# Performance work log

Hardware: AMD Instinct MI355X
Metric: run time of the kernel (lower is better)

## Reference

```python
import jax, jax.numpy as jnp
import numpy as np

G = 8            # grid_size
G2 = G * G       # total_grid_size = 64
NS = 2.0         # neighborhood_size
H = 64           # h_dim
A = 1024         # bottleneck_dim == attention_dim
S = 32           # number of sequences
N = 64           # pedestrians per sequence
P = 4096         # scene boundary points per sequence (down_samples)
B = S * N        # total batch = 2048


def setup_inputs() -> dict:
    key = jax.random.key(0)
    ks = jax.random.split(key, 16)
    starts = jnp.arange(S, dtype=jnp.int32) * N
    seq_start_end = jnp.stack([starts, starts + N], axis=1)  # (S, 2) uniform groups
    return {
        "h_states": jax.random.normal(ks[0], (1, B, H), jnp.float32),
        "end_pos": jax.random.normal(ks[1], (B, 2), jnp.float32),
        "rel_pos": jax.random.normal(ks[2], (B, 2), jnp.float32) * 0.1,
        "scene_info": jax.random.normal(ks[3], (S, P, 2), jnp.float32),
        # Attention_Decoder params (soft attention over G2 grid cells, encoder_dim=1)
        "W_enc": jax.random.normal(ks[4], (1, A), jnp.float32) * 0.05,
        "b_enc": jnp.zeros((A,), jnp.float32),
        "W_dec": jax.random.normal(ks[5], (H, A), jnp.float32) * 0.05,
        "b_dec": jnp.zeros((A,), jnp.float32),
        "w_full": jax.random.normal(ks[6], (A, 1), jnp.float32) * 0.05,
        "b_full": jnp.zeros((1,), jnp.float32),
        "W_out": jax.random.normal(ks[7], (1 + H + 4, A), jnp.float32) * 0.05,  # [ctx, h, embed_info]
        "b_out": jnp.zeros((A,), jnp.float32),
        # mlp_pool: Linear(A, A) + BatchNorm1d + ReLU
        "W_mlp": jax.random.normal(ks[8], (A, A), jnp.float32) * 0.05,
        "b_mlp": jnp.zeros((A,), jnp.float32),
        "gamma": jnp.ones((A,), jnp.float32),
        "beta": jnp.zeros((A,), jnp.float32),
        "seq_start_end": seq_start_end,
    }


def _occupancy(end_pos, scene_info, num_seqs, peds, grid_size, ns):
    """Vectorized per-pedestrian grid-cell binning + scatter-add occupancy.
    end_pos: (num_seqs*peds, 2), scene_info: (num_seqs, P, 2) -> (B, G2)."""
    g2 = grid_size * grid_size
    b = num_seqs * peds
    ep = end_pos.reshape(num_seqs, peds, 1, 2)
    sx = scene_info[:, None, :, 0]  # (S, 1, P)
    sy = scene_info[:, None, :, 1]
    tl_x = ep[..., 0] - ns / 2
    tl_y = ep[..., 1] + ns / 2
    br_x = ep[..., 0] + ns / 2
    br_y = ep[..., 1] - ns / 2
    cell_x = jnp.floor((sx - tl_x) / ns * grid_size)   # (S, N, P)
    cell_y = jnp.floor((tl_y - sy) / ns * grid_size)
    cell = (cell_x + cell_y * grid_size).astype(jnp.int32)
    # point is out-of-bound if outside the ped's neighborhood box (matches torch mask)
    oob = (sx >= br_x) | (sx <= tl_x) | (sy >= tl_y) | (sy <= br_y)
    ped = jnp.arange(b, dtype=jnp.int32).reshape(num_seqs, peds, 1)
    # torch scatters masked points into slot 0 then drops it; we use one dump slot at the end
    idx = jnp.where(oob, b * g2, ped * g2 + cell)      # (S, N, P)
    counts = jax.ops.segment_sum(
        jnp.ones(idx.size, jnp.float32), idx.reshape(-1), num_segments=b * g2 + 1)
    return counts[:-1].reshape(b, g2)


def reference(h_states, end_pos, rel_pos, scene_info,
              W_enc, b_enc, W_dec, b_dec, w_full, b_full,
              W_out, b_out, W_mlp, b_mlp, gamma, beta, seq_start_end):
    num_seqs = seq_start_end.shape[0]
    b = end_pos.shape[0]
    peds = b // num_seqs
    occ = _occupancy(end_pos, scene_info, num_seqs, peds, G, NS)   # (B, G2)
    enc = occ[..., None]                                           # (B, G2, 1)
    h = h_states.reshape(b, -1)                                    # (B, H)
    embed_info = jnp.concatenate([end_pos, rel_pos], axis=1)       # (B, 4)
    # soft attention over the G2 grid cells conditioned on the decoder hidden state
    att = jax.nn.relu(enc @ W_enc + b_enc + (h @ W_dec + b_dec)[:, None, :])  # (B, G2, A)
    e = (att @ w_full)[..., 0] + b_full                            # (B, G2)
    alpha = jax.nn.softmax(e, axis=1)
    ctx = jnp.sum(alpha[..., None] * enc, axis=1)                  # (B, 1)
    pool = jnp.concatenate([ctx, h, embed_info], axis=1) @ W_out + b_out  # (B, A)
    # mlp_pool: Linear -> BatchNorm1d (training stats, biased var) -> ReLU
    y = pool @ W_mlp + b_mlp
    mu = jnp.mean(y, axis=0)
    var = jnp.mean((y - mu) ** 2, axis=0)
    y = gamma * (y - mu) * jax.lax.rsqrt(var + 1e-5) + beta
    return jax.nn.relu(y)
```

## Files before the change

kernel.cpp:

```cpp
#include <hip/hip_runtime.h>
#include <hip/hip_bf16.h>


#define NPED 2048
#define NA   1024
#define NH   64
#define NG2  64
#define NPTS 4096

typedef unsigned short ushort_t;
typedef __attribute__((ext_vector_type(8))) short bf16x8;
typedef __attribute__((ext_vector_type(4))) float f32x4;

struct PrepPtrs { const void* p[15]; };

__device__ __forceinline__ float bf2f(ushort_t u) {
  return __uint_as_float(((unsigned int)u) << 16);
}
__device__ __forceinline__ ushort_t f2bf(float f) {
  __hip_bfloat16 b = __float2bfloat16(f);
  return *reinterpret_cast<ushort_t*>(&b);
}

__global__ void k_detect(const unsigned short* __restrict__ h, int* __restrict__ flag) {
  __shared__ int bad_sh;
  if (threadIdx.x == 0) bad_sh = 0;
  __syncthreads();
  int bad = 0;
  for (int i = threadIdx.x; i < 4096; i += 256) {
    float v = __uint_as_float(((unsigned int)h[i]) << 16);
    if (!(fabsf(v) <= 1e4f)) bad = 1;
  }
  if (bad) atomicOr(&bad_sh, 1);
  __syncthreads();
  if (threadIdx.x == 0) flag[0] = (bad_sh == 0) ? 1 : 0;
}

__device__ __forceinline__ void tp_body(const void* in, int fl, int job,
                                        int Kin, int Kpad, ushort_t* out) {
  __shared__ ushort_t t[32][40];
  int n0 = (job & 31) * 32, k0 = (job >> 5) * 32;
  int r = threadIdx.x >> 3, c4 = (threadIdx.x & 7) * 4;
  ushort4 v = make_ushort4(0, 0, 0, 0);
  if (k0 + r < Kin) {
    size_t off = (size_t)(k0 + r) * 1024 + n0 + c4;
    if (fl) {
      v = *(const ushort4*)((const ushort_t*)in + off);
    } else {
      float4 f = *(const float4*)((const float*)in + off);
      v = make_ushort4(f2bf(f.x), f2bf(f.y), f2bf(f.z), f2bf(f.w));
    }
  }
  *(ushort4*)(&t[r][c4]) = v;
  __syncthreads();
  int n = threadIdx.x >> 3, kk = (threadIdx.x & 7) * 4;
  ushort4 o = make_ushort4(t[kk][n], t[kk + 1][n], t[kk + 2][n], t[kk + 3][n]);
  *(ushort4*)(out + (size_t)(n0 + n) * Kpad + k0 + kk) = o;
}

__global__ __launch_bounds__(256) void k_prep(PrepPtrs ptrs, const int* __restrict__ flag,
                                              float* __restrict__ conv,
                                              ushort_t* __restrict__ hbf,
                                              ushort_t* __restrict__ WdecT,
                                              ushort_t* __restrict__ WoutT,
                                              ushort_t* __restrict__ WmlpT) {
  int b = blockIdx.x;
  int fl = flag[0];
  if (b < 272) {
    const int ends[11] = {4096, 8192, 270336, 271360, 272384, 273408,
                          274432, 275456, 276480, 277504, 278528};
    int idx = (b * 256 + threadIdx.x) * 4;
    int seg = 0, base = 0;
#pragma unroll
    for (int s = 0; s < 10; s++) {
      if (idx >= ends[s]) { seg = s + 1; base = ends[s]; }
    }
    int off = idx - base;
    float4 o;
    if (fl) {
      const unsigned int* src = (const unsigned int*)ptrs.p[4 + seg];
      uint2 u = *(const uint2*)(src + (off >> 1));
      o.x = __uint_as_float((u.x & 0xFFFFu) << 16);
      o.y = __uint_as_float(u.x & 0xFFFF0000u);
      o.z = __uint_as_float((u.y & 0xFFFFu) << 16);
      o.w = __uint_as_float(u.y & 0xFFFF0000u);
    } else {
      o = *(const float4*)((const float*)ptrs.p[4 + seg] + off);
    }
    *(float4*)(conv + idx) = o;
  } else if (b < 400) {
    int i = (b - 272) * 256 + threadIdx.x;
    if (fl) {
      ((ushort4*)hbf)[i] = ((const ushort4*)ptrs.p[0])[i];
    } else {
      float4 f = ((const float4*)ptrs.p[0])[i];
      ((ushort4*)hbf)[i] = make_ushort4(f2bf(f.x), f2bf(f.y), f2bf(f.z), f2bf(f.w));
    }
  } else if (b < 464) {
    tp_body(ptrs.p[1], fl, b - 400, 64, 64, WdecT);
  } else if (b < 560) {
    tp_body(ptrs.p[2], fl, b - 464, 69, 96, WoutT);
  } else {
    tp_body(ptrs.p[3], fl, b - 560, 1024, 1024, WmlpT);
  }
}

__global__ __launch_bounds__(256) void k_occupancy(const float* __restrict__ end_pos,
                                                   const float* __restrict__ scene,
                                                   float* __restrict__ occ) {
  int i = blockIdx.x;
  int s = i >> 6;
  __shared__ float cnt[NG2];
  if (threadIdx.x < NG2) cnt[threadIdx.x] = 0.0f;
  __syncthreads();
  float ex = end_pos[2 * i], ey = end_pos[2 * i + 1];
  float tlx = ex - 1.0f, tly = ey + 1.0f, brx = ex + 1.0f, bry = ey - 1.0f;
  const float2* sp = (const float2*)(scene + (size_t)s * NPTS * 2);
  for (int p = threadIdx.x; p < NPTS; p += 256) {
    float2 pt = sp[p];
    float sx = pt.x, sy = pt.y;
    bool oob = (sx >= brx) || (sx <= tlx) || (sy >= tly) || (sy <= bry);
    if (!oob) {
      int cx = (int)floorf((sx - tlx) * 0.5f * 8.0f);
      int cy = (int)floorf((tly - sy) * 0.5f * 8.0f);
      int cell = cx + cy * 8;
      if (cell >= 0 && cell < NG2) atomicAdd(&cnt[cell], 1.0f);
    }
  }
  __syncthreads();
  if (threadIdx.x < NG2) occ[i * NG2 + threadIdx.x] = cnt[threadIdx.x];
}

template <int K, int EPI>
__global__ __launch_bounds__(256) void k_mgemm(
    const ushort_t* __restrict__ A, int lda,
    const ushort_t* __restrict__ BT, int ldb,
    const float* __restrict__ bias1, const float* __restrict__ bias2,
    ushort_t* __restrict__ outb, float* __restrict__ stats) {
  __shared__ ushort_t As[64 * 32];
  __shared__ ushort_t Bs[128 * 32];
  int tid = threadIdx.x;
  int m0 = blockIdx.x * 64, n0 = blockIdx.y * 128;
  int wave = tid >> 6, lane = tid & 63, l15 = lane & 15, kg = lane >> 4;
  f32x4 acc[4][2] = {};
  int ar = tid >> 2, ag = tid & 3;
  int aswz = ag ^ ((ar >> 1) & 3);
  for (int k0 = 0; k0 < K; k0 += 32) {
    uint4 av = *(const uint4*)(A + (size_t)(m0 + ar) * lda + k0 + ag * 8);
    *(uint4*)(&As[ar * 32 + aswz * 8]) = av;
#pragma unroll
    for (int i = 0; i < 2; i++) {
      int c = tid + i * 256;
      int br = c >> 2, bg = c & 3;
      int bswz = bg ^ ((br >> 1) & 3);
      uint4 bv = *(const uint4*)(BT + (size_t)(n0 + br) * ldb + k0 + bg * 8);
      *(uint4*)(&Bs[br * 32 + bswz * 8]) = bv;
    }
    __syncthreads();
    bf16x8 af[4], bfr[2];
#pragma unroll
    for (int mt = 0; mt < 4; mt++) {
      int row = mt * 16 + l15;
      int swz = kg ^ ((row >> 1) & 3);
      af[mt] = *(const bf16x8*)(&As[row * 32 + swz * 8]);
    }
#pragma unroll
    for (int nt = 0; nt < 2; nt++) {
      int row = wave * 32 + nt * 16 + l15;
      int swz = kg ^ ((row >> 1) & 3);
      bfr[nt] = *(const bf16x8*)(&Bs[row * 32 + swz * 8]);
    }
#pragma unroll
    for (int mt = 0; mt < 4; mt++)
#pragma unroll
      for (int nt = 0; nt < 2; nt++)
        acc[mt][nt] = __builtin_amdgcn_mfma_f32_16x16x32_bf16(af[mt], bfr[nt], acc[mt][nt], 0, 0, 0);
    __syncthreads();
  }
#pragma unroll
  for (int nt = 0; nt < 2; nt++) {
    int col = n0 + wave * 32 + nt * 16 + l15;
    float bsum = (EPI == 0) ? (bias1[col] + bias2[col]) : bias1[col];
    float s1 = 0.0f, s2 = 0.0f;
#pragma unroll
    for (int mt = 0; mt < 4; mt++) {
#pragma unroll
      for (int r = 0; r < 4; r++) {
        int rowm = m0 + mt * 16 + kg * 4 + r;
        float v = acc[mt][nt][r] + bsum;
        outb[(size_t)rowm * 1024 + col] = f2bf(v);
        if (EPI == 2) { s1 += v; s2 = fmaf(v, v, s2); }
      }
    }
    if (EPI == 2) {
      s1 += __shfl_down(s1, 16); s2 += __shfl_down(s2, 16);
      s1 += __shfl_down(s1, 32); s2 += __shfl_down(s2, 32);
      if (lane < 16) {
        atomicAdd(&stats[col], s1);
        atomicAdd(&stats[1024 + col], s2);
      }
    }
  }
}

__global__ __launch_bounds__(256) void k_ectx(
    const ushort_t* __restrict__ hbf, const float* __restrict__ endp,
    const float* __restrict__ relp, const float* __restrict__ occ,
    const float* __restrict__ Wenc, const float* __restrict__ wfull,
    const ushort_t* __restrict__ hd, ushort_t* __restrict__ Xcat) {
  int wave = threadIdx.x >> 6, lane = threadIdx.x & 63;
  int p = blockIdx.x * 4 + wave;
  __shared__ float occ_sh[4][64];
  occ_sh[wave][lane] = occ[p * 64 + lane];
  float hdv[16], we[16], wf[16];
#pragma unroll
  for (int j = 0; j < 16; j++) {
    int a = lane + j * 64;
    hdv[j] = bf2f(hd[(size_t)p * 1024 + a]);
    we[j] = Wenc[a];
    wf[j] = wfull[a];
  }
  float e_mine = 0.0f;
  for (int g = 0; g < 64; g++) {
    float c = occ_sh[wave][g];
    float s = 0.0f;
#pragma unroll
    for (int j = 0; j < 16; j++)
      s += fmaxf(fmaf(c, we[j], hdv[j]), 0.0f) * wf[j];
#pragma unroll
    for (int off = 32; off > 0; off >>= 1) s += __shfl_xor(s, off);
    if (lane == g) e_mine = s;
  }
  float m = e_mine;
#pragma unroll
  for (int off = 32; off > 0; off >>= 1) m = fmaxf(m, __shfl_xor(m, off));
  float xe = __expf(e_mine - m);
  float den = xe;
#pragma unroll
  for (int off = 32; off > 0; off >>= 1) den += __shfl_xor(den, off);
  float cp = xe * occ_sh[wave][lane];
#pragma unroll
  for (int off = 32; off > 0; off >>= 1) cp += __shfl_xor(cp, off);
  float ctx = cp / den;
  size_t base = (size_t)p * 96;
  if (lane == 0) Xcat[base] = f2bf(ctx);
  Xcat[base + 1 + lane] = hbf[p * 64 + lane];
  if (lane < 2)       Xcat[base + 65 + lane] = f2bf(endp[p * 2 + lane]);
  else if (lane < 4)  Xcat[base + 67 + (lane - 2)] = f2bf(relp[p * 2 + (lane - 2)]);
  else if (lane < 31) Xcat[base + 69 + (lane - 4)] = 0;
}

__global__ void k_norm(const ushort_t* __restrict__ y_mf,
                       const float* __restrict__ stats,
                       const float* __restrict__ gamma, const float* __restrict__ beta,
                       const int* __restrict__ flag, void* __restrict__ out) {
  int idx = (blockIdx.x * 256 + threadIdx.x) * 4;
  int col = idx & (NA - 1);
  float vv[4];
#pragma unroll
  for (int j = 0; j < 4; j++) vv[j] = bf2f(y_mf[idx + j]);
  float4 s1 = *(const float4*)(stats + col);
  float4 s2 = *(const float4*)(stats + NA + col);
  float4 gm = *(const float4*)(gamma + col);
  float4 bt = *(const float4*)(beta + col);
  const float ib = 1.0f / 2048.0f;
  float m1[4] = {s1.x, s1.y, s1.z, s1.w};
  float m2[4] = {s2.x, s2.y, s2.z, s2.w};
  float gg[4] = {gm.x, gm.y, gm.z, gm.w};
  float bb[4] = {bt.x, bt.y, bt.z, bt.w};
  float o[4];
#pragma unroll
  for (int j = 0; j < 4; j++) {
    float mu = m1[j] * ib;
    float var = fmaf(-mu, mu, m2[j] * ib);
    o[j] = fmaxf(fmaf(gg[j] * (vv[j] - mu), rsqrtf(var + 1e-5f), bb[j]), 0.0f);
  }
  if (flag[0]) {
    ushort4 ov = make_ushort4(f2bf(o[0]), f2bf(o[1]), f2bf(o[2]), f2bf(o[3]));
    *(ushort4*)((ushort_t*)out + idx) = ov;
  } else {
    *(float4*)((float*)out + idx) = make_float4(o[0], o[1], o[2], o[3]);
  }
}

extern "C" void kernel_launch(void* const* d_in, const int* in_sizes, int n_in,
                              void* d_out, int out_size, void* d_ws, size_t ws_size,
                              hipStream_t stream) {
  float* ws = (float*)d_ws;
  float* conv   = ws;
  float* c_end  = conv + 0;
  float* c_rel  = conv + 4096;
  float* c_scn  = conv + 8192;
  float* c_Wenc = conv + 270336;
  float* c_benc = conv + 271360;
  float* c_bdec = conv + 272384;
  float* c_wful = conv + 273408;
  float* c_bout = conv + 274432;
  float* c_bmlp = conv + 275456;
  float* c_gam  = conv + 276480;
  float* c_bet  = conv + 277504;
  float* occ    = ws + 278528;
  float* stats  = ws + 409600;
  int*   flag   = (int*)(ws + 411648);
  ushort_t* u0    = (ushort_t*)(ws + 412672);
  ushort_t* hbf   = u0;
  ushort_t* WdecT = u0 + 131072;
  ushort_t* WoutT = u0 + 196608;
  ushort_t* WmlpT = u0 + 294912;
  ushort_t* Xcat  = u0 + 1343488;
  ushort_t* y_mf  = u0 + 1540096;
  ushort_t* hd_bf   = (ushort_t*)d_out;
  ushort_t* pool_mf = (ushort_t*)d_out;

  k_detect<<<1, 256, 0, stream>>>((const unsigned short*)d_in[0], flag);

  PrepPtrs ptrs;
  ptrs.p[0] = d_in[0];
  ptrs.p[1] = d_in[6];
  ptrs.p[2] = d_in[10];
  ptrs.p[3] = d_in[12];
  ptrs.p[4] = d_in[1];
  ptrs.p[5] = d_in[2];
  ptrs.p[6] = d_in[3];
  ptrs.p[7] = d_in[4];
  ptrs.p[8] = d_in[5];
  ptrs.p[9] = d_in[7];
  ptrs.p[10] = d_in[8];
  ptrs.p[11] = d_in[11];
  ptrs.p[12] = d_in[13];
  ptrs.p[13] = d_in[14];
  ptrs.p[14] = d_in[15];
  k_prep<<<1584, 256, 0, stream>>>(ptrs, flag, conv, hbf, WdecT, WoutT, WmlpT);

  k_occupancy<<<NPED, 256, 0, stream>>>(c_end, c_scn, occ);

  hipMemsetAsync(stats, 0, 2 * NA * sizeof(float), stream);

  k_mgemm<64, 0><<<dim3(32, 8), 256, 0, stream>>>(hbf, 64, WdecT, 64, c_benc, c_bdec,
                                                  hd_bf, nullptr);
  k_ectx<<<512, 256, 0, stream>>>(hbf, c_end, c_rel, occ, c_Wenc, c_wful, hd_bf, Xcat);
  k_mgemm<96, 1><<<dim3(32, 8), 256, 0, stream>>>(Xcat, 96, WoutT, 96, c_bout, nullptr,
                                                  pool_mf, nullptr);
  k_mgemm<1024, 2><<<dim3(32, 8), 256, 0, stream>>>(pool_mf, 1024, WmlpT, 1024, c_bmlp,
                                                    nullptr, y_mf, stats);

  k_norm<<<2048, 256, 0, stream>>>(y_mf, stats, c_gam, c_bet, flag, d_out);
}
```

Before: 175.5 us.

## Fold detection, occupancy and stats reset into prep; split pool GEMM around ctx

Drops the separate dtype-detect kernel, the occupancy kernel and the memset. Each block now derives the dtype flag itself, and occupancy binning and stats zeroing run as extra block ranges inside the prep kernel. The pool projection is split so that h and embed columns go through a GEMM run concurrently with the Wdec GEMM in one launch. The ctx column is then applied as a rank-1 update inside k_ectx, which writes the pool activations directly. This cuts launch count and serialization but adds an fp32 intermediate P1 buffer and repeated per-block flag checks.

```diff
diff --git a/kernel.cpp b/kernel.cpp
--- a/kernel.cpp
+++ b/kernel.cpp
@@ -4,7 +4,6 @@
 
 #define NPED 2048
 #define NA   1024
-#define NH   64
 #define NG2  64
 #define NPTS 4096
 
@@ -12,7 +11,7 @@
 typedef __attribute__((ext_vector_type(8))) short bf16x8;
 typedef __attribute__((ext_vector_type(4))) float f32x4;
 
-struct PrepPtrs { const void* p[15]; };
+struct PrepPtrs { const void* p[16]; };
 
 __device__ __forceinline__ float bf2f(ushort_t u) {
   return __uint_as_float(((unsigned int)u) << 16);
@@ -21,19 +20,17 @@
   __hip_bfloat16 b = __float2bfloat16(f);
   return *reinterpret_cast<ushort_t*>(&b);
 }
-
-__global__ void k_detect(const unsigned short* __restrict__ h, int* __restrict__ flag) {
+__device__ __forceinline__ int block_flag(const ushort_t* h) {
   __shared__ int bad_sh;
   if (threadIdx.x == 0) bad_sh = 0;
   __syncthreads();
-  int bad = 0;
-  for (int i = threadIdx.x; i < 4096; i += 256) {
-    float v = __uint_as_float(((unsigned int)h[i]) << 16);
-    if (!(fabsf(v) <= 1e4f)) bad = 1;
-  }
-  if (bad) atomicOr(&bad_sh, 1);
+  float v = bf2f(h[threadIdx.x & 255]);
+  if (!(fabsf(v) <= 1e4f)) atomicOr(&bad_sh, 1);
   __syncthreads();
-  if (threadIdx.x == 0) flag[0] = (bad_sh == 0) ? 1 : 0;
+  return (bad_sh == 0) ? 1 : 0;
+}
+__device__ __forceinline__ float lde(const void* p, size_t i, int fl) {
+  return fl ? bf2f(((const ushort_t*)p)[i]) : ((const float*)p)[i];
 }
 
 __device__ __forceinline__ void tp_body(const void* in, int fl, int job,
@@ -58,21 +55,24 @@
   *(ushort4*)(out + (size_t)(n0 + n) * Kpad + k0 + kk) = o;
 }
 
-__global__ __launch_bounds__(256) void k_prep(PrepPtrs ptrs, const int* __restrict__ flag,
+__global__ __launch_bounds__(256) void k_prep(PrepPtrs ptrs,
                                               float* __restrict__ conv,
                                               ushort_t* __restrict__ hbf,
                                               ushort_t* __restrict__ WdecT,
                                               ushort_t* __restrict__ WoutT,
-                                              ushort_t* __restrict__ WmlpT) {
+                                              ushort_t* __restrict__ WmlpT,
+                                              ushort_t* __restrict__ Xcat0,
+                                              float* __restrict__ occ,
+                                              float* __restrict__ stats) {
   int b = blockIdx.x;
-  int fl = flag[0];
-  if (b < 272) {
-    const int ends[11] = {4096, 8192, 270336, 271360, 272384, 273408,
-                          274432, 275456, 276480, 277504, 278528};
+  int fl = block_flag((const ushort_t*)ptrs.p[0]);
+  if (b < 273) {
+    const int ends[12] = {4096, 8192, 270336, 271360, 272384, 273408,
+                          274432, 275456, 276480, 277504, 278528, 279552};
     int idx = (b * 256 + threadIdx.x) * 4;
     int seg = 0, base = 0;
 #pragma unroll
-    for (int s = 0; s < 10; s++) {
+    for (int s = 0; s < 11; s++) {
       if (idx >= ends[s]) { seg = s + 1; base = ends[s]; }
     }
     int off = idx - base;
@@ -88,57 +88,76 @@
       o = *(const float4*)((const float*)ptrs.p[4 + seg] + off);
     }
     *(float4*)(conv + idx) = o;
-  } else if (b < 400) {
-    int i = (b - 272) * 256 + threadIdx.x;
+  } else if (b < 401) {
+    int i = (b - 273) * 256 + threadIdx.x;
     if (fl) {
       ((ushort4*)hbf)[i] = ((const ushort4*)ptrs.p[0])[i];
     } else {
       float4 f = ((const float4*)ptrs.p[0])[i];
       ((ushort4*)hbf)[i] = make_ushort4(f2bf(f.x), f2bf(f.y), f2bf(f.z), f2bf(f.w));
     }
-  } else if (b < 464) {
-    tp_body(ptrs.p[1], fl, b - 400, 64, 64, WdecT);
-  } else if (b < 560) {
-    tp_body(ptrs.p[2], fl, b - 464, 69, 96, WoutT);
+  } else if (b < 465) {
+    tp_body(ptrs.p[1], fl, b - 401, 64, 64, WdecT);
+  } else if (b < 561) {
+    const void* wout1 = fl ? (const void*)((const ushort_t*)ptrs.p[2] + 1024)
+                           : (const void*)((const float*)ptrs.p[2] + 1024);
+    tp_body(wout1, fl, b - 465, 68, 96, WoutT);
+  } else if (b < 1585) {
+    tp_body(ptrs.p[3], fl, b - 561, 1024, 1024, WmlpT);
+  } else if (b < 1777) {
+    int flat = (b - 1585) * 256 + threadIdx.x;
+    int e4 = flat * 4;
+    int r = e4 / 96, c = e4 - r * 96;
+    ushort4 v = make_ushort4(0, 0, 0, 0);
+    if (c < 64) {
+      if (fl) v = *(const ushort4*)((const ushort_t*)ptrs.p[0] + r * 64 + c);
+      else {
+        float4 f = *(const float4*)((const float*)ptrs.p[0] + r * 64 + c);
+        v = make_ushort4(f2bf(f.x), f2bf(f.y), f2bf(f.z), f2bf(f.w));
+      }
+    } else if (c == 64) {
+      v.x = f2bf(lde(ptrs.p[4], 2 * r, fl));
+      v.y = f2bf(lde(ptrs.p[4], 2 * r + 1, fl));
+      v.z = f2bf(lde(ptrs.p[5], 2 * r, fl));
+      v.w = f2bf(lde(ptrs.p[5], 2 * r + 1, fl));
+    }
+    *(ushort4*)(Xcat0 + e4) = v;
+  } else if (b < 3825) {
+    int i = b - 1777;
+    int s = i >> 6;
+    __shared__ float cnt[NG2];
+    if (threadIdx.x < NG2) cnt[threadIdx.x] = 0.0f;
+    __syncthreads();
+    float ex = lde(ptrs.p[4], 2 * i, fl), ey = lde(ptrs.p[4], 2 * i + 1, fl);
+    float tlx = ex - 1.0f, tly = ey + 1.0f, brx = ex + 1.0f, bry = ey - 1.0f;
+    const void* scn = ptrs.p[6];
+    for (int p = threadIdx.x; p < NPTS; p += 256) {
+      size_t o2 = (size_t)s * NPTS * 2 + 2 * p;
+      float sx = lde(scn, o2, fl), sy = lde(scn, o2 + 1, fl);
+      bool oob = (sx >= brx) || (sx <= tlx) || (sy >= tly) || (sy <= bry);
+      if (!oob) {
+        int cx = (int)floorf((sx - tlx) * 0.5f * 8.0f);
+        int cy = (int)floorf((tly - sy) * 0.5f * 8.0f);
+        int cell = cx + cy * 8;
+        if (cell >= 0 && cell < NG2) atomicAdd(&cnt[cell], 1.0f);
+      }
+    }
+    __syncthreads();
+    if (threadIdx.x < NG2) occ[i * NG2 + threadIdx.x] = cnt[threadIdx.x];
   } else {
-    tp_body(ptrs.p[3], fl, b - 560, 1024, 1024, WmlpT);
-  }
-}
-
-__global__ __launch_bounds__(256) void k_occupancy(const float* __restrict__ end_pos,
-                                                   const float* __restrict__ scene,
-                                                   float* __restrict__ occ) {
-  int i = blockIdx.x;
-  int s = i >> 6;
-  __shared__ float cnt[NG2];
-  if (threadIdx.x < NG2) cnt[threadIdx.x] = 0.0f;
-  __syncthreads();
-  float ex = end_pos[2 * i], ey = end_pos[2 * i + 1];
-  float tlx = ex - 1.0f, tly = ey + 1.0f, brx = ex + 1.0f, bry = ey - 1.0f;
-  const float2* sp = (const float2*)(scene + (size_t)s * NPTS * 2);
-  for (int p = threadIdx.x; p < NPTS; p += 256) {
-    float2 pt = sp[p];
-    float sx = pt.x, sy = pt.y;
-    bool oob = (sx >= brx) || (sx <= tlx) || (sy >= tly) || (sy <= bry);
-    if (!oob) {
-      int cx = (int)floorf((sx - tlx) * 0.5f * 8.0f);
-      int cy = (int)floorf((tly - sy) * 0.5f * 8.0f);
-      int cell = cx + cy * 8;
-      if (cell >= 0 && cell < NG2) atomicAdd(&cnt[cell], 1.0f);
-    }
-  }
-  __syncthreads();
-  if (threadIdx.x < NG2) occ[i * NG2 + threadIdx.x] = cnt[threadIdx.x];
+#pragma unroll
+    for (int k = 0; k < 8; k++) stats[threadIdx.x + 256 * k] = 0.0f;
+  }
 }
 
 template <int K, int EPI>
-__global__ __launch_bounds__(256) void k_mgemm(
+__device__ __forceinline__ void mgemm_body(
+    ushort_t* As, ushort_t* Bs,
     const ushort_t* __restrict__ A, int lda,
     const ushort_t* __restrict__ BT, int ldb,
     const float* __restrict__ bias1, const float* __restrict__ bias2,
-    ushort_t* __restrict__ outb, float* __restrict__ stats) {
-  __shared__ ushort_t As[64 * 32];
-  __shared__ ushort_t Bs[128 * 32];
+    ushort_t* __restrict__ outb, float* __restrict__ outf,
+    float* __restrict__ stats) {
   int tid = threadIdx.x;
   int m0 = blockIdx.x * 64, n0 = blockIdx.y * 128;
   int wave = tid >> 6, lane = tid & 63, l15 = lane & 15, kg = lane >> 4;
@@ -188,7 +207,8 @@
       for (int r = 0; r < 4; r++) {
         int rowm = m0 + mt * 16 + kg * 4 + r;
         float v = acc[mt][nt][r] + bsum;
-        outb[(size_t)rowm * 1024 + col] = f2bf(v);
+        if (EPI == 3) outf[(size_t)rowm * 1024 + col] = v;
+        else outb[(size_t)rowm * 1024 + col] = f2bf(v);
         if (EPI == 2) { s1 += v; s2 = fmaf(v, v, s2); }
       }
     }
@@ -203,11 +223,34 @@
   }
 }
 
+__global__ __launch_bounds__(256) void k_gemm2(
+    const ushort_t* __restrict__ hbf, const ushort_t* __restrict__ WdecT,
+    const float* __restrict__ benc, const float* __restrict__ bdec,
+    ushort_t* __restrict__ hd_out,
+    const ushort_t* __restrict__ Xcat0, const ushort_t* __restrict__ WoutT,
+    const float* __restrict__ bout, float* __restrict__ P1) {
+  __shared__ ushort_t As[64 * 32];
+  __shared__ ushort_t Bs[128 * 32];
+  if (blockIdx.z == 0)
+    mgemm_body<64, 0>(As, Bs, hbf, 64, WdecT, 64, benc, bdec, hd_out, nullptr, nullptr);
+  else
+    mgemm_body<96, 3>(As, Bs, Xcat0, 96, WoutT, 96, bout, nullptr, nullptr, P1, nullptr);
+}
+
+__global__ __launch_bounds__(256) void k_mgemm_y(
+    const ushort_t* __restrict__ A, const ushort_t* __restrict__ BT,
+    const float* __restrict__ bias1, ushort_t* __restrict__ outb,
+    float* __restrict__ stats) {
+  __shared__ ushort_t As[64 * 32];
+  __shared__ ushort_t Bs[128 * 32];
+  mgemm_body<1024, 2>(As, Bs, A, 1024, BT, 1024, bias1, nullptr, outb, nullptr, stats);
+}
+
 __global__ __launch_bounds__(256) void k_ectx(
-    const ushort_t* __restrict__ hbf, const float* __restrict__ endp,
-    const float* __restrict__ relp, const float* __restrict__ occ,
+    const float* __restrict__ occ,
     const float* __restrict__ Wenc, const float* __restrict__ wfull,
-    const ushort_t* __restrict__ hd, ushort_t* __restrict__ Xcat) {
+    const float* __restrict__ w0, const float* __restrict__ P1,
+    const ushort_t* __restrict__ hd, ushort_t* __restrict__ pool) {
   int wave = threadIdx.x >> 6, lane = threadIdx.x & 63;
   int p = blockIdx.x * 4 + wave;
   __shared__ float occ_sh[4][64];
@@ -242,18 +285,18 @@
 #pragma unroll
   for (int off = 32; off > 0; off >>= 1) cp += __shfl_xor(cp, off);
   float ctx = cp / den;
-  size_t base = (size_t)p * 96;
-  if (lane == 0) Xcat[base] = f2bf(ctx);
-  Xcat[base + 1 + lane] = hbf[p * 64 + lane];
-  if (lane < 2)       Xcat[base + 65 + lane] = f2bf(endp[p * 2 + lane]);
-  else if (lane < 4)  Xcat[base + 67 + (lane - 2)] = f2bf(relp[p * 2 + (lane - 2)]);
-  else if (lane < 31) Xcat[base + 69 + (lane - 4)] = 0;
+#pragma unroll
+  for (int j = 0; j < 16; j++) {
+    int a = lane + j * 64;
+    pool[(size_t)p * 1024 + a] = f2bf(fmaf(ctx, w0[a], P1[(size_t)p * 1024 + a]));
+  }
 }
 
 __global__ void k_norm(const ushort_t* __restrict__ y_mf,
                        const float* __restrict__ stats,
                        const float* __restrict__ gamma, const float* __restrict__ beta,
-                       const int* __restrict__ flag, void* __restrict__ out) {
+                       const ushort_t* __restrict__ hsrc, void* __restrict__ out) {
+  int fl = block_flag(hsrc);
   int idx = (blockIdx.x * 256 + threadIdx.x) * 4;
   int col = idx & (NA - 1);
   float vv[4];
@@ -275,7 +318,7 @@
     float var = fmaf(-mu, mu, m2[j] * ib);
     o[j] = fmaxf(fmaf(gg[j] * (vv[j] - mu), rsqrtf(var + 1e-5f), bb[j]), 0.0f);
   }
-  if (flag[0]) {
+  if (fl) {
     ushort4 ov = make_ushort4(f2bf(o[0]), f2bf(o[1]), f2bf(o[2]), f2bf(o[3]));
     *(ushort4*)((ushort_t*)out + idx) = ov;
   } else {
@@ -288,9 +331,6 @@
                               hipStream_t stream) {
   float* ws = (float*)d_ws;
   float* conv   = ws;
-  float* c_end  = conv + 0;
-  float* c_rel  = conv + 4096;
-  float* c_scn  = conv + 8192;
   float* c_Wenc = conv + 270336;
   float* c_benc = conv + 271360;
   float* c_bdec = conv + 272384;
@@ -299,20 +339,19 @@
   float* c_bmlp = conv + 275456;
   float* c_gam  = conv + 276480;
   float* c_bet  = conv + 277504;
-  float* occ    = ws + 278528;
-  float* stats  = ws + 409600;
-  int*   flag   = (int*)(ws + 411648);
-  ushort_t* u0    = (ushort_t*)(ws + 412672);
+  float* c_w0   = conv + 278528;
+  float* occ    = ws + 280576;
+  float* stats  = ws + 411648;
+  float* P1     = ws + 413696;
+  ushort_t* u0    = (ushort_t*)(ws + 2510848);
   ushort_t* hbf   = u0;
   ushort_t* WdecT = u0 + 131072;
   ushort_t* WoutT = u0 + 196608;
   ushort_t* WmlpT = u0 + 294912;
-  ushort_t* Xcat  = u0 + 1343488;
+  ushort_t* Xcat0 = u0 + 1343488;
   ushort_t* y_mf  = u0 + 1540096;
   ushort_t* hd_bf   = (ushort_t*)d_out;
   ushort_t* pool_mf = (ushort_t*)d_out;
-
-  k_detect<<<1, 256, 0, stream>>>((const unsigned short*)d_in[0], flag);
 
   PrepPtrs ptrs;
   ptrs.p[0] = d_in[0];
@@ -330,19 +369,18 @@
   ptrs.p[12] = d_in[13];
   ptrs.p[13] = d_in[14];
   ptrs.p[14] = d_in[15];
-  k_prep<<<1584, 256, 0, stream>>>(ptrs, flag, conv, hbf, WdecT, WoutT, WmlpT);
-
-  k_occupancy<<<NPED, 256, 0, stream>>>(c_end, c_scn, occ);
-
-  hipMemsetAsync(stats, 0, 2 * NA * sizeof(float), stream);
-
-  k_mgemm<64, 0><<<dim3(32, 8), 256, 0, stream>>>(hbf, 64, WdecT, 64, c_benc, c_bdec,
-                                                  hd_bf, nullptr);
-  k_ectx<<<512, 256, 0, stream>>>(hbf, c_end, c_rel, occ, c_Wenc, c_wful, hd_bf, Xcat);
-  k_mgemm<96, 1><<<dim3(32, 8), 256, 0, stream>>>(Xcat, 96, WoutT, 96, c_bout, nullptr,
-                                                  pool_mf, nullptr);
-  k_mgemm<1024, 2><<<dim3(32, 8), 256, 0, stream>>>(pool_mf, 1024, WmlpT, 1024, c_bmlp,
-                                                    nullptr, y_mf, stats);
-
-  k_norm<<<2048, 256, 0, stream>>>(y_mf, stats, c_gam, c_bet, flag, d_out);
-}
+  ptrs.p[15] = d_in[10];
+
+  k_prep<<<3826, 256, 0, stream>>>(ptrs, conv, hbf, WdecT, WoutT, WmlpT,
+                                   Xcat0, occ, stats);
+
+  k_gemm2<<<dim3(32, 8, 2), 256, 0, stream>>>(hbf, WdecT, c_benc, c_bdec, hd_bf,
+                                              Xcat0, WoutT, c_bout, P1);
+
+  k_ectx<<<512, 256, 0, stream>>>(occ, c_Wenc, c_wful, c_w0, P1, hd_bf, pool_mf);
+
+  k_mgemm_y<<<dim3(32, 8), 256, 0, stream>>>(pool_mf, WmlpT, c_bmlp, y_mf, stats);
+
+  k_norm<<<2048, 256, 0, stream>>>(y_mf, stats, c_gam, c_bet,
+                                   (const ushort_t*)d_in[0], d_out);
+}
```

Result: faster. 163.6 us (-6.8%).
